# Kernel optimization log

Hardware: AMD Instinct MI355X
Metric: run time of the kernel (lower is better)

The kernel has to match this reference:

```python
import jax, jax.numpy as jnp
import numpy as np

N = 50000          # number of points
C = 64             # num_clusters (embedding width)
K_RAD = 32         # radius graph max_num_neighbors
K_KNN = 10         # knn graph k


def setup_inputs() -> dict:
    key = jax.random.key(0)
    ks = jax.random.split(key, 8)
    x0 = jax.random.normal(ks[0], (N, 3), jnp.float32)
    pos0 = jax.random.normal(ks[1], (N, 3), jnp.float32)
    # R0/t0 come from rigid_fitting in the original (external helper); use
    # orthonormal matrices from batched QR as realistic per-point rotations.
    A = jax.random.normal(ks[2], (N, 3, 3), jnp.float32)
    R0, _ = jnp.linalg.qr(A)
    t0 = jax.random.normal(ks[3], (N, 3), jnp.float32) * 0.1
    # pool1 k=1 assignment: point i -> cluster assign01[i]
    assign01 = jax.random.randint(ks[4], (N,), 0, C, dtype=jnp.int32)
    # radius graph edges (source, target): each point has K_RAD neighbors
    radius_src = jax.random.randint(ks[5], (N * K_RAD,), 0, N, dtype=jnp.int32)
    radius_dst = jnp.repeat(jnp.arange(N, dtype=jnp.int32), K_RAD)
    # knn-10 graph edges used by WeightedAvg
    knn_src = jax.random.randint(ks[6], (N * K_KNN,), 0, N, dtype=jnp.int32)
    knn_dst = jnp.repeat(jnp.arange(N, dtype=jnp.int32), K_KNN)
    return dict(x0=x0, pos0=pos0, R0=R0, t0=t0, assign01=assign01,
                radius_src=radius_src, radius_dst=radius_dst,
                knn_src=knn_src, knn_dst=knn_dst)


def _rigid_layer(xfeat, pos0, x0, R0, t0, src, dst):
    # RigidPropModule.message + max aggregation (nn=None, lin1: w=-1, b=0.01)
    Ri = R0[dst]                     # [E,3,3] target-side rotation
    ti = t0[dst]                     # [E,3]
    posj = pos0[src]                 # [E,3]
    xj = x0[src]                     # [E,3]
    pred = jnp.einsum('eij,ej->ei', Ri, posj) + ti
    d = jnp.sum((pred - xj) ** 2, axis=-1, keepdims=True)   # [E,1]
    w = jax.nn.sigmoid(-d + 0.01)
    msg = w * xfeat[src]             # [E,C]
    agg = jax.ops.segment_max(msg, dst, num_segments=xfeat.shape[0])
    # messages are non-negative; nodes with no edges get 0 (torch_scatter fill)
    return jnp.maximum(agg, 0.0)


def reference(x0, pos0, R0, t0, assign01, radius_src, radius_dst, knn_src, knn_dst):
    n = x0.shape[0]
    # scatter_add of one-hot cluster embeddings back to points
    emb = jnp.zeros((n, C), jnp.float32).at[jnp.arange(n), assign01].add(1.0)
    m1 = _rigid_layer(emb, pos0, x0, R0, t0, radius_src, radius_dst)
    m2 = _rigid_layer(m1, pos0, x0, R0, t0, radius_src, radius_dst)
    m3 = _rigid_layer(m2, pos0, x0, R0, t0, radius_src, radius_dst)
    m4 = _rigid_layer(m2, pos0, x0, R0, t0, radius_src, radius_dst)
    m5 = _rigid_layer(m2, pos0, x0, R0, t0, radius_src, radius_dst)
    msg = jnp.stack([m1.sum(-1), m2.sum(-1), m3.sum(-1),
                     m4.sum(-1), m5.sum(-1)], axis=-1)      # [N,5]
    # predictor: Linear(5,1) with w=ones, b=-17, then sigmoid
    conf = jax.nn.sigmoid(msg.sum(-1, keepdims=True) - 17.0)  # [N,1]
    # WeightedAvg over knn edges: out[t] = sum_s conf[s]*val[s] / sum_s conf[s]
    cw = conf[knn_src]                                       # [E,1]
    num_R = jax.ops.segment_sum(cw * R0.reshape(n, 9)[knn_src], knn_dst, num_segments=n)
    num_t = jax.ops.segment_sum(cw * t0[knn_src], knn_dst, num_segments=n)
    den = jax.ops.segment_sum(cw, knn_dst, num_segments=n) + 1e-8
    R_out = (num_R / den).reshape(n, 3, 3)
    t_out = num_t / den
    x_out = jnp.einsum('nij,nj->ni', R_out, pos0) + t_out
    return x_out, R_out, t_out
```

## Files before the change

kernel.cpp:

```cpp
#include <hip/hip_runtime.h>
#include <hip/hip_fp16.h>
#include <math.h>

#define N_PTS 50000
#define C_DIM 64
#define K_RAD 32
#define K_KNN 10
#define E_RAD (N_PTS * K_RAD)

__device__ inline __half2 hmax2(__half2 a, __half2 b) {
    __half2 d;
    asm("v_pk_max_f16 %0, %1, %2" : "=v"(d) : "v"(a), "v"(b));
    return d;
}

__device__ inline __half2 shfl_xor_h2(__half2 v, int mask) {
    int i = *(int*)&v;
    int r = __shfl_xor(i, mask);
    return *(__half2*)&r;
}

__global__ void pack_tables_kernel(const float* __restrict__ pos0,
                                   const float* __restrict__ x0,
                                   const int* __restrict__ assign,
                                   float4* __restrict__ geo) {
    int i = blockIdx.x * blockDim.x + threadIdx.x;
    if (i >= N_PTS) return;
    geo[i * 2 + 0] = make_float4(pos0[3 * i], pos0[3 * i + 1], pos0[3 * i + 2], x0[3 * i]);
    geo[i * 2 + 1] = make_float4(x0[3 * i + 1], x0[3 * i + 2], __int_as_float(assign[i]), 0.0f);
}

__global__ void ew_layer1_kernel(const float4* __restrict__ geo,
                                 const float* __restrict__ R0,
                                 const float* __restrict__ t0,
                                 const int* __restrict__ src,
                                 unsigned int* __restrict__ packed,
                                 __half* __restrict__ m1,
                                 float* __restrict__ sum1,
                                 float4* __restrict__ rt4) {
    __shared__ int lm[16][C_DIM];
    __shared__ float ldsR[16 * 9];
    __shared__ float ldsT[16 * 3];
    int tid = threadIdx.x;
    int blk = blockIdx.x;
    ((int*)lm)[tid] = 0;
    ((int*)lm)[tid + 256] = 0;
    ((int*)lm)[tid + 512] = 0;
    ((int*)lm)[tid + 768] = 0;
    if (tid < 144) ldsR[tid] = R0[blk * 144 + tid];
    if (tid < 48) ldsT[tid] = t0[blk * 48 + tid];
    int nl = tid >> 4;
    int ng = blk * 16 + nl;
    int e0 = tid & 15, e1 = e0 + 16;
    int s0 = src[ng * K_RAD + e0];
    int s1 = src[ng * K_RAD + e1];
    float4 g0a = geo[s0 * 2 + 0];
    float4 g0b = geo[s0 * 2 + 1];
    float4 g1a = geo[s1 * 2 + 0];
    float4 g1b = geo[s1 * 2 + 1];
    __syncthreads();
    if (tid < 48) {
        int n = tid / 3, slot = tid % 3;
        const float* R = ldsR + n * 9;
        const float* T = ldsT + n * 3;
        float4 q;
        if (slot == 0) q = make_float4(R[0], R[1], R[2], R[3]);
        else if (slot == 1) q = make_float4(R[4], R[5], R[6], R[7]);
        else q = make_float4(R[8], T[0], T[1], T[2]);
        rt4[(blk * 16 + n) * 4 + slot] = q;
    }
    const float* R = ldsR + nl * 9;
    const float* T = ldsT + nl * 3;
    float r0 = R[0] * g0a.x + R[1] * g0a.y + R[2] * g0a.z + T[0] - g0a.w;
    float r1 = R[3] * g0a.x + R[4] * g0a.y + R[5] * g0a.z + T[1] - g0b.x;
    float r2 = R[6] * g0a.x + R[7] * g0a.y + R[8] * g0a.z + T[2] - g0b.y;
    float d0 = r0 * r0 + r1 * r1 + r2 * r2;
    float w0 = 1.0f / (1.0f + __expf(d0 - 0.01f));
    float u0 = R[0] * g1a.x + R[1] * g1a.y + R[2] * g1a.z + T[0] - g1a.w;
    float u1 = R[3] * g1a.x + R[4] * g1a.y + R[5] * g1a.z + T[1] - g1b.x;
    float u2 = R[6] * g1a.x + R[7] * g1a.y + R[8] * g1a.z + T[2] - g1b.y;
    float d1 = u0 * u0 + u1 * u1 + u2 * u2;
    float w1 = 1.0f / (1.0f + __expf(d1 - 0.01f));
    packed[ng * K_RAD + e0] =
        ((unsigned int)s0 << 16) | (unsigned int)__half_as_ushort(__float2half_rn(w0));
    packed[ng * K_RAD + e1] =
        ((unsigned int)s1 << 16) | (unsigned int)__half_as_ushort(__float2half_rn(w1));
    atomicMax(&lm[nl][__float_as_int(g0b.z)], __float_as_int(w0));
    atomicMax(&lm[nl][__float_as_int(g1b.z)], __float_as_int(w1));
    __syncthreads();
    int c0 = (tid & 15) * 4;
    float v0 = __int_as_float(lm[nl][c0 + 0]);
    float v1 = __int_as_float(lm[nl][c0 + 1]);
    float v2 = __int_as_float(lm[nl][c0 + 2]);
    float v3 = __int_as_float(lm[nl][c0 + 3]);
    __half2 h01 = __floats2half2_rn(v0, v1);
    __half2 h23 = __floats2half2_rn(v2, v3);
    uint2 uo = make_uint2(*(unsigned int*)&h01, *(unsigned int*)&h23);
    *(uint2*)(m1 + ng * C_DIM + c0) = uo;
    float s = v0 + v1 + v2 + v3;
    s += __shfl_down(s, 8);
    s += __shfl_down(s, 4);
    s += __shfl_down(s, 2);
    s += __shfl_down(s, 1);
    if ((tid & 15) == 0) sum1[ng] = s;
}

__global__ void layer_pk_kernel(const unsigned int* __restrict__ packed,
                                const __half* __restrict__ xin,
                                __half* __restrict__ xout,
                                float* __restrict__ sum_out) {
    int gid = blockIdx.x * blockDim.x + threadIdx.x;
    int lane = gid & 63;
    int node = (gid >> 6) * 2 + (lane >> 5);
    int eslot = (lane >> 3) & 3;
    int cpos = lane & 7;
    const uint4* pk4 = (const uint4*)(packed + node * K_RAD + eslot * 8);
    uint4 q0 = pk4[0], q1 = pk4[1];
    unsigned int pes[8] = {q0.x, q0.y, q0.z, q0.w, q1.x, q1.y, q1.z, q1.w};
    __half2 a0 = __float2half2_rn(0.0f), a1 = a0, a2 = a0, a3 = a0;
#pragma unroll
    for (int p = 0; p < 8; ++p) {
        unsigned int pe = pes[p];
        float4 f = *(const float4*)(xin + (pe >> 16) * C_DIM + cpos * 8);
        __half2* h = (__half2*)&f;
        __half2 w2 = __half2half2(__ushort_as_half((unsigned short)(pe & 0xffffu)));
        a0 = hmax2(a0, __hmul2(w2, h[0]));
        a1 = hmax2(a1, __hmul2(w2, h[1]));
        a2 = hmax2(a2, __hmul2(w2, h[2]));
        a3 = hmax2(a3, __hmul2(w2, h[3]));
    }
#pragma unroll
    for (int off = 8; off <= 16; off <<= 1) {
        a0 = hmax2(a0, shfl_xor_h2(a0, off));
        a1 = hmax2(a1, shfl_xor_h2(a1, off));
        a2 = hmax2(a2, shfl_xor_h2(a2, off));
        a3 = hmax2(a3, shfl_xor_h2(a3, off));
    }
    if (eslot == 0) {
        float4 o;
        __half2* oh = (__half2*)&o;
        oh[0] = a0; oh[1] = a1; oh[2] = a2; oh[3] = a3;
        ((float4*)(xout + node * C_DIM))[cpos] = o;
    }
    float2 v0 = __half22float2(a0), v1 = __half22float2(a1);
    float2 v2 = __half22float2(a2), v3 = __half22float2(a3);
    float s = v0.x + v0.y + v1.x + v1.y + v2.x + v2.y + v3.x + v3.y;
    s += __shfl_xor(s, 1);
    s += __shfl_xor(s, 2);
    s += __shfl_xor(s, 4);
    if ((lane & 31) == 0) sum_out[node] = s;
}

__global__ void layer3_conf_pk_kernel(const unsigned int* __restrict__ packed,
                                      const __half* __restrict__ xin,
                                      const float* __restrict__ sum1,
                                      const float* __restrict__ sum2,
                                      float* __restrict__ rt4f) {
    int gid = blockIdx.x * blockDim.x + threadIdx.x;
    int lane = gid & 63;
    int node = (gid >> 6) * 2 + (lane >> 5);
    int eslot = (lane >> 3) & 3;
    int cpos = lane & 7;
    const uint4* pk4 = (const uint4*)(packed + node * K_RAD + eslot * 8);
    uint4 q0 = pk4[0], q1 = pk4[1];
    unsigned int pes[8] = {q0.x, q0.y, q0.z, q0.w, q1.x, q1.y, q1.z, q1.w};
    __half2 a0 = __float2half2_rn(0.0f), a1 = a0, a2 = a0, a3 = a0;
#pragma unroll
    for (int p = 0; p < 8; ++p) {
        unsigned int pe = pes[p];
        float4 f = *(const float4*)(xin + (pe >> 16) * C_DIM + cpos * 8);
        __half2* h = (__half2*)&f;
        __half2 w2 = __half2half2(__ushort_as_half((unsigned short)(pe & 0xffffu)));
        a0 = hmax2(a0, __hmul2(w2, h[0]));
        a1 = hmax2(a1, __hmul2(w2, h[1]));
        a2 = hmax2(a2, __hmul2(w2, h[2]));
        a3 = hmax2(a3, __hmul2(w2, h[3]));
    }
#pragma unroll
    for (int off = 8; off <= 16; off <<= 1) {
        a0 = hmax2(a0, shfl_xor_h2(a0, off));
        a1 = hmax2(a1, shfl_xor_h2(a1, off));
        a2 = hmax2(a2, shfl_xor_h2(a2, off));
        a3 = hmax2(a3, shfl_xor_h2(a3, off));
    }
    float2 v0 = __half22float2(a0), v1 = __half22float2(a1);
    float2 v2 = __half22float2(a2), v3 = __half22float2(a3);
    float s = v0.x + v0.y + v1.x + v1.y + v2.x + v2.y + v3.x + v3.y;
    s += __shfl_xor(s, 1);
    s += __shfl_xor(s, 2);
    s += __shfl_xor(s, 4);
    if ((lane & 31) == 0) {
        float tot = sum1[node] + sum2[node] + 3.0f * s - 17.0f;
        rt4f[node * 16 + 12] = 1.0f / (1.0f + __expf(-tot));
    }
}

__global__ void wavg_kernel(const int* __restrict__ knn_src,
                            const float4* __restrict__ rt4,
                            const float* __restrict__ pos0,
                            float* __restrict__ out) {
    int gid = blockIdx.x * blockDim.x + threadIdx.x;
    int lane = gid & 63;
    int t = (gid >> 6) * 16 + (lane >> 2);
    int part = lane & 3;
    if (t >= N_PTS) return;
    float4 acc = make_float4(0.f, 0.f, 0.f, 0.f);
    for (int j = 0; j < K_KNN; ++j) {
        int s = knn_src[t * K_KNN + j];
        float4 q = rt4[s * 4 + part];
        float c = __shfl(q.x, lane | 3);
        if (part == 3) {
            acc.x += c;
        } else {
            acc.x += c * q.x; acc.y += c * q.y;
            acc.z += c * q.z; acc.w += c * q.w;
        }
    }
    float den = __shfl(acc.x, lane | 3) + 1e-8f;
    float inv = 1.0f / den;
    float4 sc = make_float4(acc.x * inv, acc.y * inv, acc.z * inv, acc.w * inv);
    int base = lane & ~3;
    float R3 = __shfl(sc.w, base + 0);
    float R6 = __shfl(sc.z, base + 1);
    float R7 = __shfl(sc.w, base + 1);
    float t0v = __shfl(sc.y, base + 2);
    float t1v = __shfl(sc.z, base + 2);
    float px = pos0[t * 3 + 0], py = pos0[t * 3 + 1], pz = pos0[t * 3 + 2];
    float* Rout = out + N_PTS * 3;
    float* tout = out + N_PTS * 12;
    if (part == 0) {
        out[t * 3 + 0] = sc.x * px + sc.y * py + sc.z * pz + t0v;
        Rout[t * 9 + 0] = sc.x; Rout[t * 9 + 1] = sc.y;
        Rout[t * 9 + 2] = sc.z; Rout[t * 9 + 3] = sc.w;
    } else if (part == 1) {
        out[t * 3 + 1] = R3 * px + sc.x * py + sc.y * pz + t1v;
        Rout[t * 9 + 4] = sc.x; Rout[t * 9 + 5] = sc.y;
        Rout[t * 9 + 6] = sc.z; Rout[t * 9 + 7] = sc.w;
    } else if (part == 2) {
        out[t * 3 + 2] = R6 * px + R7 * py + sc.x * pz + sc.w;
        Rout[t * 9 + 8] = sc.x;
        tout[t * 3 + 0] = sc.y; tout[t * 3 + 1] = sc.z; tout[t * 3 + 2] = sc.w;
    }
}

extern "C" void kernel_launch(void* const* d_in, const int* in_sizes, int n_in,
                              void* d_out, int out_size, void* d_ws, size_t ws_size,
                              hipStream_t stream) {
    const float* x0 = (const float*)d_in[0];
    const float* pos0 = (const float*)d_in[1];
    const float* R0 = (const float*)d_in[2];
    const float* t0 = (const float*)d_in[3];
    const int* assign01 = (const int*)d_in[4];
    const int* radius_src = (const int*)d_in[5];
    const int* knn_src = (const int*)d_in[7];

    char* ws = (char*)d_ws;
    unsigned int* packed = (unsigned int*)ws;
    __half* mA = (__half*)(ws + 6400000);
    __half* mB = (__half*)(ws + 12800000);
    float4* geo = (float4*)(ws + 19200000);
    float4* rt4 = (float4*)(ws + 20800000);
    float* sum1 = (float*)(ws + 24000000);
    float* sum2 = (float*)(ws + 24200000);
    float* out = (float*)d_out;

    pack_tables_kernel<<<(N_PTS + 255) / 256, 256, 0, stream>>>(
        pos0, x0, assign01, geo);

    ew_layer1_kernel<<<N_PTS / 16, 256, 0, stream>>>(
        geo, R0, t0, radius_src, packed, mA, sum1, rt4);

    layer_pk_kernel<<<N_PTS / 8, 256, 0, stream>>>(
        packed, mA, mB, sum2);

    layer3_conf_pk_kernel<<<N_PTS / 8, 256, 0, stream>>>(
        packed, mB, sum1, sum2, (float*)rt4);

    wavg_kernel<<<(N_PTS * 4 + 255) / 256, 256, 0, stream>>>(
        knn_src, rt4, pos0, out);
}
```

Baseline: 136.4 us.

## Split feature matrix into two 32-channel planes and restructure gather layers

Stores the fp16 layer features as two planes of 32 channels each, so each gather kernel handles one plane per block and the working set per pass is halved for better cache reuse. Each thread now issues four independent gathers up front instead of eight serially dependent ones. Per-node partial sums now go into spare slots of the rt4 table, and a new conf_kernel combines them. wavg also splits each node's 10 neighbours across two lane groups with all loads hoisted for more memory parallelism. The cost is one extra kernel launch and double the per-node packed-edge reads, since both planes reread the edge list.

```diff
diff --git a/kernel.cpp b/kernel.cpp
--- a/kernel.cpp
+++ b/kernel.cpp
@@ -7,6 +7,7 @@
 #define K_RAD 32
 #define K_KNN 10
 #define E_RAD (N_PTS * K_RAD)
+#define NGRP (N_PTS / 8)
 
 __device__ inline __half2 hmax2(__half2 a, __half2 b) {
     __half2 d;
@@ -36,11 +37,11 @@
                                  const int* __restrict__ src,
                                  unsigned int* __restrict__ packed,
                                  __half* __restrict__ m1,
-                                 float* __restrict__ sum1,
                                  float4* __restrict__ rt4) {
     __shared__ int lm[16][C_DIM];
     __shared__ float ldsR[16 * 9];
     __shared__ float ldsT[16 * 3];
+    float* rt4f = (float*)rt4;
     int tid = threadIdx.x;
     int blk = blockIdx.x;
     ((int*)lm)[tid] = 0;
@@ -61,12 +62,12 @@
     __syncthreads();
     if (tid < 48) {
         int n = tid / 3, slot = tid % 3;
-        const float* R = ldsR + n * 9;
-        const float* T = ldsT + n * 3;
+        const float* Rp = ldsR + n * 9;
+        const float* Tp = ldsT + n * 3;
         float4 q;
-        if (slot == 0) q = make_float4(R[0], R[1], R[2], R[3]);
-        else if (slot == 1) q = make_float4(R[4], R[5], R[6], R[7]);
-        else q = make_float4(R[8], T[0], T[1], T[2]);
+        if (slot == 0) q = make_float4(Rp[0], Rp[1], Rp[2], Rp[3]);
+        else if (slot == 1) q = make_float4(Rp[4], Rp[5], Rp[6], Rp[7]);
+        else q = make_float4(Rp[8], Tp[0], Tp[1], Tp[2]);
         rt4[(blk * 16 + n) * 4 + slot] = q;
     }
     const float* R = ldsR + nl * 9;
@@ -96,41 +97,50 @@
     __half2 h01 = __floats2half2_rn(v0, v1);
     __half2 h23 = __floats2half2_rn(v2, v3);
     uint2 uo = make_uint2(*(unsigned int*)&h01, *(unsigned int*)&h23);
-    *(uint2*)(m1 + ng * C_DIM + c0) = uo;
+    int plane = c0 >> 5;
+    int ci = c0 & 31;
+    *(uint2*)(m1 + plane * (N_PTS * 32) + ng * 32 + ci) = uo;
     float s = v0 + v1 + v2 + v3;
     s += __shfl_down(s, 8);
     s += __shfl_down(s, 4);
     s += __shfl_down(s, 2);
     s += __shfl_down(s, 1);
-    if ((tid & 15) == 0) sum1[ng] = s;
+    if ((tid & 15) == 0) rt4f[ng * 16 + 12] = s - 17.0f;
 }
 
 __global__ void layer_pk_kernel(const unsigned int* __restrict__ packed,
                                 const __half* __restrict__ xin,
                                 __half* __restrict__ xout,
-                                float* __restrict__ sum_out) {
-    int gid = blockIdx.x * blockDim.x + threadIdx.x;
-    int lane = gid & 63;
-    int node = (gid >> 6) * 2 + (lane >> 5);
-    int eslot = (lane >> 3) & 3;
-    int cpos = lane & 7;
-    const uint4* pk4 = (const uint4*)(packed + node * K_RAD + eslot * 8);
-    uint4 q0 = pk4[0], q1 = pk4[1];
-    unsigned int pes[8] = {q0.x, q0.y, q0.z, q0.w, q1.x, q1.y, q1.z, q1.w};
+                                float* __restrict__ rt4f) {
+    int blk = blockIdx.x;
+    int plane = (blk & 7) >> 2;
+    int grp = (blk >> 3) * 4 + (blk & 3);
+    if (grp >= NGRP) return;
+    int tid = threadIdx.x;
+    int lane = tid & 63;
+    int node = grp * 8 + (tid >> 6) * 2 + (lane >> 5);
+    int hl = lane & 31;
+    int eslot = hl >> 2;
+    int cpos = lane & 3;
+    const __half* xp = xin + plane * (N_PTS * 32);
+    uint4 pk = *(const uint4*)(packed + node * K_RAD + eslot * 4);
+    unsigned int pes[4] = {pk.x, pk.y, pk.z, pk.w};
+    float4 f[4];
+#pragma unroll
+    for (int p = 0; p < 4; ++p)
+        f[p] = *(const float4*)(xp + (pes[p] >> 16) * 32 + cpos * 8);
     __half2 a0 = __float2half2_rn(0.0f), a1 = a0, a2 = a0, a3 = a0;
 #pragma unroll
-    for (int p = 0; p < 8; ++p) {
-        unsigned int pe = pes[p];
-        float4 f = *(const float4*)(xin + (pe >> 16) * C_DIM + cpos * 8);
-        __half2* h = (__half2*)&f;
-        __half2 w2 = __half2half2(__ushort_as_half((unsigned short)(pe & 0xffffu)));
+    for (int p = 0; p < 4; ++p) {
+        __half2* h = (__half2*)&f[p];
+        __half2 w2 = __half2half2(__ushort_as_half((unsigned short)(pes[p] & 0xffffu)));
         a0 = hmax2(a0, __hmul2(w2, h[0]));
         a1 = hmax2(a1, __hmul2(w2, h[1]));
         a2 = hmax2(a2, __hmul2(w2, h[2]));
         a3 = hmax2(a3, __hmul2(w2, h[3]));
     }
 #pragma unroll
-    for (int off = 8; off <= 16; off <<= 1) {
+    for (int off = 4; off <= 16; off <<= 1) {
         a0 = hmax2(a0, shfl_xor_h2(a0, off));
         a1 = hmax2(a1, shfl_xor_h2(a1, off));
         a2 = hmax2(a2, shfl_xor_h2(a2, off));
@@ -140,44 +150,49 @@
         float4 o;
         __half2* oh = (__half2*)&o;
         oh[0] = a0; oh[1] = a1; oh[2] = a2; oh[3] = a3;
-        ((float4*)(xout + node * C_DIM))[cpos] = o;
+        *(float4*)(xout + plane * (N_PTS * 32) + node * 32 + cpos * 8) = o;
     }
     float2 v0 = __half22float2(a0), v1 = __half22float2(a1);
     float2 v2 = __half22float2(a2), v3 = __half22float2(a3);
     float s = v0.x + v0.y + v1.x + v1.y + v2.x + v2.y + v3.x + v3.y;
     s += __shfl_xor(s, 1);
     s += __shfl_xor(s, 2);
-    s += __shfl_xor(s, 4);
-    if ((lane & 31) == 0) sum_out[node] = s;
-}
-
-__global__ void layer3_conf_pk_kernel(const unsigned int* __restrict__ packed,
+    if (hl == 0) rt4f[node * 16 + 13 + plane] = s;
+}
+
+__global__ void layer3_partial_kernel(const unsigned int* __restrict__ packed,
                                       const __half* __restrict__ xin,
-                                      const float* __restrict__ sum1,
-                                      const float* __restrict__ sum2,
-                                      float* __restrict__ rt4f) {
-    int gid = blockIdx.x * blockDim.x + threadIdx.x;
-    int lane = gid & 63;
-    int node = (gid >> 6) * 2 + (lane >> 5);
-    int eslot = (lane >> 3) & 3;
-    int cpos = lane & 7;
-    const uint4* pk4 = (const uint4*)(packed + node * K_RAD + eslot * 8);
-    uint4 q0 = pk4[0], q1 = pk4[1];
-    unsigned int pes[8] = {q0.x, q0.y, q0.z, q0.w, q1.x, q1.y, q1.z, q1.w};
+                                      float* __restrict__ rt4f,
+                                      float* __restrict__ sum3b) {
+    int blk = blockIdx.x;
+    int plane = (blk & 7) >> 2;
+    int grp = (blk >> 3) * 4 + (blk & 3);
+    if (grp >= NGRP) return;
+    int tid = threadIdx.x;
+    int lane = tid & 63;
+    int node = grp * 8 + (tid >> 6) * 2 + (lane >> 5);
+    int hl = lane & 31;
+    int eslot = hl >> 2;
+    int cpos = lane & 3;
+    const __half* xp = xin + plane * (N_PTS * 32);
+    uint4 pk = *(const uint4*)(packed + node * K_RAD + eslot * 4);
+    unsigned int pes[4] = {pk.x, pk.y, pk.z, pk.w};
+    float4 f[4];
+#pragma unroll
+    for (int p = 0; p < 4; ++p)
+        f[p] = *(const float4*)(xp + (pes[p] >> 16) * 32 + cpos * 8);
     __half2 a0 = __float2half2_rn(0.0f), a1 = a0, a2 = a0, a3 = a0;
 #pragma unroll
-    for (int p = 0; p < 8; ++p) {
-        unsigned int pe = pes[p];
-        float4 f = *(const float4*)(xin + (pe >> 16) * C_DIM + cpos * 8);
-        __half2* h = (__half2*)&f;
-        __half2 w2 = __half2half2(__ushort_as_half((unsigned short)(pe & 0xffffu)));
+    for (int p = 0; p < 4; ++p) {
+        __half2* h = (__half2*)&f[p];
+        __half2 w2 = __half2half2(__ushort_as_half((unsigned short)(pes[p] & 0xffffu)));
         a0 = hmax2(a0, __hmul2(w2, h[0]));
         a1 = hmax2(a1, __hmul2(w2, h[1]));
         a2 = hmax2(a2, __hmul2(w2, h[2]));
         a3 = hmax2(a3, __hmul2(w2, h[3]));
     }
 #pragma unroll
-    for (int off = 8; off <= 16; off <<= 1) {
+    for (int off = 4; off <= 16; off <<= 1) {
         a0 = hmax2(a0, shfl_xor_h2(a0, off));
         a1 = hmax2(a1, shfl_xor_h2(a1, off));
         a2 = hmax2(a2, shfl_xor_h2(a2, off));
@@ -188,11 +203,19 @@
     float s = v0.x + v0.y + v1.x + v1.y + v2.x + v2.y + v3.x + v3.y;
     s += __shfl_xor(s, 1);
     s += __shfl_xor(s, 2);
-    s += __shfl_xor(s, 4);
-    if ((lane & 31) == 0) {
-        float tot = sum1[node] + sum2[node] + 3.0f * s - 17.0f;
-        rt4f[node * 16 + 12] = 1.0f / (1.0f + __expf(-tot));
-    }
+    if (hl == 0) {
+        if (plane == 0) rt4f[node * 16 + 15] = s;
+        else            sum3b[node] = s;
+    }
+}
+
+__global__ void conf_kernel(float* __restrict__ rt4f,
+                            const float* __restrict__ sum3b) {
+    int n = blockIdx.x * blockDim.x + threadIdx.x;
+    if (n >= N_PTS) return;
+    float4 v = *(const float4*)(rt4f + n * 16 + 12);
+    float tot = v.x + v.y + v.z + 3.0f * (v.w + sum3b[n]);
+    rt4f[n * 16 + 12] = 1.0f / (1.0f + __expf(-tot));
 }
 
 __global__ void wavg_kernel(const int* __restrict__ knn_src,
@@ -201,21 +224,31 @@
                             float* __restrict__ out) {
     int gid = blockIdx.x * blockDim.x + threadIdx.x;
     int lane = gid & 63;
-    int t = (gid >> 6) * 16 + (lane >> 2);
+    int t = gid >> 3;
     int part = lane & 3;
+    int half = (lane >> 2) & 1;
     if (t >= N_PTS) return;
+    int ids[5];
+#pragma unroll
+    for (int k = 0; k < 5; ++k) ids[k] = knn_src[t * K_KNN + half * 5 + k];
+    float4 q[5];
+#pragma unroll
+    for (int k = 0; k < 5; ++k) q[k] = rt4[ids[k] * 4 + part];
     float4 acc = make_float4(0.f, 0.f, 0.f, 0.f);
-    for (int j = 0; j < K_KNN; ++j) {
-        int s = knn_src[t * K_KNN + j];
-        float4 q = rt4[s * 4 + part];
-        float c = __shfl(q.x, lane | 3);
+#pragma unroll
+    for (int k = 0; k < 5; ++k) {
+        float c = __shfl(q[k].x, lane | 3);
         if (part == 3) {
             acc.x += c;
         } else {
-            acc.x += c * q.x; acc.y += c * q.y;
-            acc.z += c * q.z; acc.w += c * q.w;
+            acc.x += c * q[k].x; acc.y += c * q[k].y;
+            acc.z += c * q[k].z; acc.w += c * q[k].w;
         }
     }
+    acc.x += __shfl_xor(acc.x, 4);
+    acc.y += __shfl_xor(acc.y, 4);
+    acc.z += __shfl_xor(acc.z, 4);
+    acc.w += __shfl_xor(acc.w, 4);
     float den = __shfl(acc.x, lane | 3) + 1e-8f;
     float inv = 1.0f / den;
     float4 sc = make_float4(acc.x * inv, acc.y * inv, acc.z * inv, acc.w * inv);
@@ -225,21 +258,23 @@
     float R7 = __shfl(sc.w, base + 1);
     float t0v = __shfl(sc.y, base + 2);
     float t1v = __shfl(sc.z, base + 2);
-    float px = pos0[t * 3 + 0], py = pos0[t * 3 + 1], pz = pos0[t * 3 + 2];
-    float* Rout = out + N_PTS * 3;
-    float* tout = out + N_PTS * 12;
-    if (part == 0) {
-        out[t * 3 + 0] = sc.x * px + sc.y * py + sc.z * pz + t0v;
-        Rout[t * 9 + 0] = sc.x; Rout[t * 9 + 1] = sc.y;
-        Rout[t * 9 + 2] = sc.z; Rout[t * 9 + 3] = sc.w;
-    } else if (part == 1) {
-        out[t * 3 + 1] = R3 * px + sc.x * py + sc.y * pz + t1v;
-        Rout[t * 9 + 4] = sc.x; Rout[t * 9 + 5] = sc.y;
-        Rout[t * 9 + 6] = sc.z; Rout[t * 9 + 7] = sc.w;
-    } else if (part == 2) {
-        out[t * 3 + 2] = R6 * px + R7 * py + sc.x * pz + sc.w;
-        Rout[t * 9 + 8] = sc.x;
-        tout[t * 3 + 0] = sc.y; tout[t * 3 + 1] = sc.z; tout[t * 3 + 2] = sc.w;
+    if (half == 0) {
+        float px = pos0[t * 3 + 0], py = pos0[t * 3 + 1], pz = pos0[t * 3 + 2];
+        float* Rout = out + N_PTS * 3;
+        float* tout = out + N_PTS * 12;
+        if (part == 0) {
+            out[t * 3 + 0] = sc.x * px + sc.y * py + sc.z * pz + t0v;
+            Rout[t * 9 + 0] = sc.x; Rout[t * 9 + 1] = sc.y;
+            Rout[t * 9 + 2] = sc.z; Rout[t * 9 + 3] = sc.w;
+        } else if (part == 1) {
+            out[t * 3 + 1] = R3 * px + sc.x * py + sc.y * pz + t1v;
+            Rout[t * 9 + 4] = sc.x; Rout[t * 9 + 5] = sc.y;
+            Rout[t * 9 + 6] = sc.z; Rout[t * 9 + 7] = sc.w;
+        } else if (part == 2) {
+            out[t * 3 + 2] = R6 * px + R7 * py + sc.x * pz + sc.w;
+            Rout[t * 9 + 8] = sc.x;
+            tout[t * 3 + 0] = sc.y; tout[t * 3 + 1] = sc.z; tout[t * 3 + 2] = sc.w;
+        }
     }
 }
 
@@ -260,22 +295,24 @@
     __half* mB = (__half*)(ws + 12800000);
     float4* geo = (float4*)(ws + 19200000);
     float4* rt4 = (float4*)(ws + 20800000);
-    float* sum1 = (float*)(ws + 24000000);
-    float* sum2 = (float*)(ws + 24200000);
+    float* sum3b = (float*)(ws + 24000000);
     float* out = (float*)d_out;
 
     pack_tables_kernel<<<(N_PTS + 255) / 256, 256, 0, stream>>>(
         pos0, x0, assign01, geo);
 
     ew_layer1_kernel<<<N_PTS / 16, 256, 0, stream>>>(
-        geo, R0, t0, radius_src, packed, mA, sum1, rt4);
-
-    layer_pk_kernel<<<N_PTS / 8, 256, 0, stream>>>(
-        packed, mA, mB, sum2);
-
-    layer3_conf_pk_kernel<<<N_PTS / 8, 256, 0, stream>>>(
-        packed, mB, sum1, sum2, (float*)rt4);
-
-    wavg_kernel<<<(N_PTS * 4 + 255) / 256, 256, 0, stream>>>(
+        geo, R0, t0, radius_src, packed, mA, rt4);
+
+    layer_pk_kernel<<<1563 * 8, 256, 0, stream>>>(
+        packed, mA, mB, (float*)rt4);
+
+    layer3_partial_kernel<<<1563 * 8, 256, 0, stream>>>(
+        packed, mB, (float*)rt4, sum3b);
+
+    conf_kernel<<<(N_PTS + 255) / 256, 256, 0, stream>>>(
+        (float*)rt4, sum3b);
+
+    wavg_kernel<<<(N_PTS * 8 + 255) / 256, 256, 0, stream>>>(
         knn_src, rt4, pos0, out);
 }
```

Measured after the change: 138.8 us. Within noise of the previous version (+1.8%).
